# Kernel optimization log

Hardware: AMD Instinct MI355X
Metric: run time of the kernel (lower is better)

The kernel has to match this reference:

```python
import jax, jax.numpy as jnp
import numpy as np

N, D, E = 100000, 128, 1600000
C = 1.0
MIN_NORM = 1e-15   # hgcn min_norm clamp
BALL_EPS = 4e-3    # float32 eps for proj onto Poincare ball


def artanh(x):
    # hgcn Artanh clamps input away from +-1 (use 1e-7, the fp32-representable analog of 1e-15)
    return jnp.arctanh(jnp.clip(x, -1.0 + 1e-7, 1.0 - 1e-7))


def _norm(x):
    return jnp.maximum(jnp.linalg.norm(x, axis=-1, keepdims=True), MIN_NORM)


def proj(x, c):
    norm = _norm(x)
    maxnorm = (1.0 - BALL_EPS) / jnp.sqrt(c)
    return jnp.where(norm > maxnorm, x / norm * maxnorm, x)


def expmap0(u, c):
    sc = jnp.sqrt(c)
    n = _norm(u)
    return jnp.tanh(sc * n) * u / (sc * n)


def logmap0(p, c):
    sc = jnp.sqrt(c)
    n = _norm(p)
    return artanh(sc * n) * p / (sc * n)


def mobius_add(x, y, c):
    x2 = jnp.sum(x * x, -1, keepdims=True)
    y2 = jnp.sum(y * y, -1, keepdims=True)
    xy = jnp.sum(x * y, -1, keepdims=True)
    num = (1.0 + 2.0 * c * xy + c * y2) * x + (1.0 - c * x2) * y
    den = 1.0 + 2.0 * c * xy + c * c * x2 * y2
    return num / jnp.maximum(den, MIN_NORM)


def mobius_matvec(m, x, c):
    sc = jnp.sqrt(c)
    xn = _norm(x)
    mx = x @ m.T
    mxn = _norm(mx)
    res = jnp.tanh(mxn / xn * artanh(sc * xn)) * mx / (mxn * sc)
    zero = jnp.all(mx == 0, axis=-1, keepdims=True)
    return jnp.where(zero, jnp.zeros_like(res), res)


def hgc_layer(x, edge_index, edge_weight, w, b, c_in, c_out, n):
    # HypLinear: mobius matvec + hyperbolic bias
    h = proj(mobius_matvec(w, x, c_in), c_in)
    hyp_b = proj(expmap0(b[None, :], c_in), c_in)
    h = proj(mobius_add(h, hyp_b, c_in), c_in)
    # HypAgg: aggregate in tangent space via sparse adjacency (spmm)
    xt = logmap0(h, c_in)                                   # [N, D]
    msg = xt[edge_index[1]] * edge_weight[:, None]          # [E, D]
    agg = jax.ops.segment_sum(msg, edge_index[0], num_segments=n)
    h = proj(expmap0(agg, c_in), c_in)
    # HypAct: relu in tangent space, re-map to ball at c_out
    xt = jax.nn.relu(logmap0(h, c_in))
    return proj(expmap0(xt, c_out), c_out)


def setup_inputs() -> dict:
    key = jax.random.key(0)
    ks = jax.random.split(key, 8)
    x = jax.random.normal(ks[0], (N, D), dtype=jnp.float32)
    edge_index = jax.random.randint(ks[1], (2, E), 0, N, dtype=jnp.int64 if jax.config.jax_enable_x64 else jnp.int32)
    edge_weight = jax.random.uniform(ks[2], (E,), dtype=jnp.float32)
    s = 1.0 / np.sqrt(D)
    w1 = jax.random.normal(ks[3], (D, D), dtype=jnp.float32) * s
    b1 = jax.random.normal(ks[4], (D,), dtype=jnp.float32) * s
    w2 = jax.random.normal(ks[5], (D, D), dtype=jnp.float32) * s
    b2 = jax.random.normal(ks[6], (D,), dtype=jnp.float32) * s
    return {"x": x, "edge_index": edge_index, "edge_weight": edge_weight,
            "w1": w1, "b1": b1, "w2": w2, "b2": b2}


def reference(x, edge_index, edge_weight, w1, b1, w2, b2):
    c = jnp.float32(C)
    n = x.shape[0]
    # encode(): proj_tan0 is identity on the Poincare ball
    xh = proj(expmap0(x, c), c)
    h = hgc_layer(xh, edge_index, edge_weight, w1, b1, c, c, n)
    h = hgc_layer(h, edge_index, edge_weight, w2, b2, c, c, n)
    return h
```

## Files before the change

### kernel.cpp

```cpp
#include <hip/hip_runtime.h>
#include <math.h>
#include <stdint.h>

#define D 128
#define MAXNORM (1.0f - 4e-3f)
#define ART_CLAMP 0.9999999f
#define BKT_BITS 7
#define BKT_NODES 128
#define BKT_CAP 4096

typedef __attribute__((ext_vector_type(8))) short short8;
typedef __attribute__((ext_vector_type(4))) float float4v;
typedef __attribute__((ext_vector_type(4))) int intv4;

__device__ __forceinline__ float waveAllReduce(float v) {
#pragma unroll
    for (int off = 32; off; off >>= 1) v += __shfl_xor(v, off, 64);
    return v;
}

__device__ __forceinline__ float reduce16(float v) {
    v += __shfl_xor(v, 8, 64);
    v += __shfl_xor(v, 4, 64);
    v += __shfl_xor(v, 2, 64);
    v += __shfl_xor(v, 1, 64);
    return v;
}

__device__ __forceinline__ uint16_t f2bf(float f) {
    uint32_t u = __float_as_uint(f);
    uint32_t r = u + 0x7FFFu + ((u >> 16) & 1u);
    return (uint16_t)(r >> 16);
}
__device__ __forceinline__ float bf2f(uint16_t b) {
    return __uint_as_float((uint32_t)b << 16);
}

__device__ __forceinline__ float rcpf(float x) { return __builtin_amdgcn_rcpf(x); }
__device__ __forceinline__ float fsqrtf(float x) { return __builtin_amdgcn_sqrtf(x); }
__device__ __forceinline__ float fast_tanh(float x) {
    float e = __expf(2.0f * x);
    float t = 1.0f - 2.0f * rcpf(e + 1.0f);
    return (x < 1e-4f) ? x : t;
}
__device__ __forceinline__ float fast_atanh(float x) {
    float t = 0.5f * __logf((1.0f + x) * rcpf(1.0f - x));
    return (x < 1e-4f) ? x : t;
}


__global__ __launch_bounds__(64) void biasKernel(const float* __restrict__ B1,
                                                 const float* __restrict__ B2,
                                                 float* __restrict__ HBOUT) {
    int lane = threadIdx.x;
    const float* B = blockIdx.x ? B2 : B1;
    float v0 = B[lane], v1 = B[lane + 64];
    float nn = fmaxf(sqrtf(waveAllReduce(v0 * v0 + v1 * v1)), 1e-15f);
    float t = tanhf(nn);
    float sc = t / nn;
    float pn = fmaxf(t, 1e-15f);
    if (pn > MAXNORM) sc *= MAXNORM / pn;
    HBOUT[blockIdx.x * D + lane] = v0 * sc;
    HBOUT[blockIdx.x * D + lane + 64] = v1 * sc;
}


__global__ __launch_bounds__(256) void prepW(const float* __restrict__ W1,
                                             const float* __restrict__ W2,
                                             uint16_t* __restrict__ Whi1,
                                             uint16_t* __restrict__ Wlo1,
                                             uint16_t* __restrict__ Whi2,
                                             uint16_t* __restrict__ Wlo2) {
    int i = blockIdx.x * 256 + threadIdx.x;
    float a1 = W1[i];
    uint16_t h1 = f2bf(a1);
    Whi1[i] = h1;
    Wlo1[i] = f2bf(a1 - bf2f(h1));
    float a2 = W2[i];
    uint16_t h2 = f2bf(a2);
    Whi2[i] = h2;
    Wlo2[i] = f2bf(a2 - bf2f(h2));
}


__global__ __launch_bounds__(256) void rowNorms(const float* __restrict__ X,
                                                float* __restrict__ XN, int n) {
    int lane = threadIdx.x & 63;
    int wv = (blockIdx.x * 256 + threadIdx.x) >> 6;
    int nw = (gridDim.x * 256) >> 6;
    for (int r = wv; r < n; r += nw) {
        float2 v = *(const float2*)(X + (size_t)r * D + lane * 2);
        float nn = sqrtf(waveAllReduce(v.x * v.x + v.y * v.y));
        if (lane == 0) XN[r] = nn;
    }
}


__global__ __launch_bounds__(256) void bucketHisto(const int* __restrict__ DST,
                                                   int* __restrict__ bcnt, int E, int B) {
    __shared__ int cnt[1024];
    int tid = threadIdx.x;
    for (int i = tid; i < B; i += 256) cnt[i] = 0;
    __syncthreads();
    int start = blockIdx.x * 8192;
    int endE = min(start + 8192, E);
    for (int e = start + tid; e < endE; e += 256)
        atomicAdd(&cnt[DST[e] >> BKT_BITS], 1);
    __syncthreads();
    for (int i = tid; i < B; i += 256)
        if (cnt[i]) atomicAdd(&bcnt[i], cnt[i]);
}

__global__ __launch_bounds__(1024) void bucketScan(const int* __restrict__ bcnt,
                                                   int* __restrict__ boff,
                                                   int* __restrict__ gcur,
                                                   int* __restrict__ rp_last,
                                                   int B, int E) {
    __shared__ int sd[1024];
    int tid = threadIdx.x;
    int v = (tid < B) ? bcnt[tid] : 0;
    sd[tid] = v;
    __syncthreads();
    for (int off = 1; off < 1024; off <<= 1) {
        int t = (tid >= off) ? sd[tid - off] : 0;
        __syncthreads();
        sd[tid] += t;
        __syncthreads();
    }
    int ex = sd[tid] - v;
    if (tid < B) { boff[tid] = ex; gcur[tid] = ex; }
    if (tid == 0) { boff[B] = E; *rp_last = E; }
}

__global__ __launch_bounds__(256) void binEdges(const int* __restrict__ DST,
                                                const int* __restrict__ SRC,
                                                const float* __restrict__ EW,
                                                int* __restrict__ gcur,
                                                int2* __restrict__ binned, int E, int B) {
    __shared__ int cnt[1024];
    __shared__ int base[1024];
    int tid = threadIdx.x;
    int start = blockIdx.x * 8192;
    int endE = min(start + 8192, E);
    for (int i = tid; i < B; i += 256) cnt[i] = 0;
    __syncthreads();
    for (int e = start + tid; e < endE; e += 256)
        atomicAdd(&cnt[DST[e] >> BKT_BITS], 1);
    __syncthreads();
    for (int i = tid; i < B; i += 256) {
        int c = cnt[i];
        base[i] = (c > 0) ? atomicAdd(&gcur[i], c) : 0;
        cnt[i] = 0;
    }
    __syncthreads();
    for (int e = start + tid; e < endE; e += 256) {
        int d = DST[e];
        int bk = d >> BKT_BITS;
        int r = atomicAdd(&cnt[bk], 1);
        binned[base[bk] + r] =
            make_int2(SRC[e] | ((d & (BKT_NODES - 1)) << 24), __float_as_int(EW[e]));
    }
}


__global__ __launch_bounds__(256) void perBucketSort(int2* __restrict__ binned,
                                                     const int* __restrict__ boff,
                                                     int* __restrict__ rp, int n) {
    __shared__ int cnt[BKT_NODES];
    __shared__ int cur[BKT_NODES];
    __shared__ int2 buf[BKT_CAP];
    int tid = threadIdx.x;
    int b = blockIdx.x;
    int beg = boff[b], end = boff[b + 1];

    if (tid < BKT_NODES) cnt[tid] = 0;
    __syncthreads();
    for (int e = beg + tid; e < end; e += 256)
        atomicAdd(&cnt[((uint32_t)binned[e].x) >> 24], 1);
    __syncthreads();
    int v = (tid < BKT_NODES) ? cnt[tid] : 0;
    if (tid < BKT_NODES) cur[tid] = v;
    __syncthreads();
    for (int off = 1; off < BKT_NODES; off <<= 1) {
        int t = (tid < BKT_NODES && tid >= off) ? cur[tid - off] : 0;
        __syncthreads();
        if (tid < BKT_NODES) cur[tid] += t;
        __syncthreads();
    }
    if (tid < BKT_NODES) {
        int ex = cur[tid] - v;
        int g = b * BKT_NODES + tid;
        if (g < n) rp[g] = beg + ex;
        cur[tid] = ex;
    }
    __syncthreads();
    for (int e = beg + tid; e < end; e += 256) {
        int2 pr = binned[e];
        int dl = ((uint32_t)pr.x) >> 24;
        int pos = atomicAdd(&cur[dl], 1);
        if (pos < BKT_CAP) buf[pos] = make_int2(pr.x & 0x00FFFFFF, pr.y);
    }
    __syncthreads();
    int cnt_tot = end - beg;
    for (int i = tid; i < cnt_tot && i < BKT_CAP; i += 256)
        binned[beg + i] = buf[i];
}


__device__ __forceinline__ void split8(const float* v, short8* hi, short8* lo) {
    union { uint32_t u[4]; short8 s; } H, L;
#pragma unroll
    for (int i = 0; i < 4; i++) {
        uint16_t h0 = f2bf(v[2 * i]), h1 = f2bf(v[2 * i + 1]);
        uint16_t l0 = f2bf(v[2 * i] - bf2f(h0));
        uint16_t l1 = f2bf(v[2 * i + 1] - bf2f(h1));
        H.u[i] = (uint32_t)h0 | ((uint32_t)h1 << 16);
        L.u[i] = (uint32_t)l0 | ((uint32_t)l1 << 16);
    }
    *hi = H.s;
    *lo = L.s;
}

#define CS_STRIDE 136

template <bool ENCODE>
__global__ __launch_bounds__(256, 3) void gemmM(const float* __restrict__ A,
                                                const uint16_t* __restrict__ Whi,
                                                const uint16_t* __restrict__ Wlo,
                                                const float* __restrict__ XN,
                                                const float* __restrict__ HB,
                                                uint16_t* __restrict__ XT, int n) {
    __shared__ short8 Ah[2][16][16];
    __shared__ short8 Al[2][16][16];
    __shared__ float Cs[16 * CS_STRIDE];
    int tid = threadIdx.x;
    int lane = tid & 63;
    int wv = tid >> 6;
    int tx = lane & 15;
    int q = lane >> 4;
    int sw = tx & 7;
    int row0 = blockIdx.x * 64;

    short8 wh[2][4], wl[2][4];
#pragma unroll
    for (int c = 0; c < 2; c++) {
        int wrow = 16 * (2 * wv + c) + tx;
        const uint16_t* ph = Whi + (size_t)wrow * D + q * 8;
        const uint16_t* pl = Wlo + (size_t)wrow * D + q * 8;
#pragma unroll
        for (int t = 0; t < 4; t++) {
            wh[c][t] = *(const short8*)(ph + t * 32);
            wl[c][t] = *(const short8*)(pl + t * 32);
        }
    }

    float hbf[8];
#pragma unroll
    for (int c = 0; c < 8; c++) hbf[c] = HB[16 * c + tx];
    float hbsq = 0.f;
#pragma unroll
    for (int c = 0; c < 8; c++) hbsq += hbf[c] * hbf[c];
    float hb2 = reduce16(hbsq);

    auto loadA = [&](int tau, float4& v0, float4& v1) {
        int gr = row0 + tau * 16 + tx;
        if (gr >= n) gr = n - 1;
        const float4* ap = (const float4*)(A + (size_t)gr * D + wv * 32 + q * 8);
        v0 = ap[0];
        v1 = ap[1];
    };
    auto splitStore = [&](int b, float4 v0, float4 v1) {
        float v[8] = {v0.x, v0.y, v0.z, v0.w, v1.x, v1.y, v1.z, v1.w};
        short8 hi, lo;
        split8(v, &hi, &lo);
        int pch = (4 * wv + q) ^ sw;
        Ah[b][tx][pch] = hi;
        Al[b][tx][pch] = lo;
    };

    float4 pa0, pa1;
    loadA(0, pa0, pa1);
    splitStore(0, pa0, pa1);
    loadA(1, pa0, pa1);
    __syncthreads();

#pragma unroll
    for (int tau = 0; tau < 4; tau++) {
        int b = tau & 1;
        float4v acc[2];
        acc[0] = (float4v){0.f, 0.f, 0.f, 0.f};
        acc[1] = (float4v){0.f, 0.f, 0.f, 0.f};
#pragma unroll
        for (int t = 0; t < 4; t++) {
            int pch = (4 * t + q) ^ sw;
            short8 ahi = Ah[b][tx][pch];
            short8 alo = Al[b][tx][pch];
#pragma unroll
            for (int c = 0; c < 2; c++) {
                acc[c] = __builtin_amdgcn_mfma_f32_16x16x32_bf16(ahi, wh[c][t], acc[c], 0, 0, 0);
                acc[c] = __builtin_amdgcn_mfma_f32_16x16x32_bf16(ahi, wl[c][t], acc[c], 0, 0, 0);
                acc[c] = __builtin_amdgcn_mfma_f32_16x16x32_bf16(alo, wh[c][t], acc[c], 0, 0, 0);
            }
        }

#pragma unroll
        for (int c = 0; c < 2; c++) {
            int col = 16 * (2 * wv + c) + tx;
#pragma unroll
            for (int p = 0; p < 4; p++) {
                int lr = 4 * q + p;
                Cs[lr * CS_STRIDE + ((col + 4 * lr) & 127)] = acc[c][p];
            }
        }

        if (tau < 3) {
            splitStore(b ^ 1, pa0, pa1);
            if (tau < 2) loadA(tau + 2, pa0, pa1);
        }
        __syncthreads();

        int lr = 4 * wv + q;
        int row = row0 + tau * 16 + lr;
        if (row < n) {
            float y[8];
#pragma unroll
            for (int c = 0; c < 8; c++)
                y[c] = Cs[lr * CS_STRIDE + ((16 * c + tx + 4 * lr) & 127)];

            float s = 0.f;
#pragma unroll
            for (int c = 0; c < 8; c++) s += y[c] * y[c];
            float yn2 = reduce16(s);
            float sc, xns;
            if (ENCODE) {
                float nn = fmaxf(XN[row], 1e-15f);
                float t = fast_tanh(nn);
                sc = t * rcpf(nn);
                float pn = fmaxf(t, 1e-15f);
                if (pn > MAXNORM) { sc *= MAXNORM * rcpf(pn); pn = MAXNORM; }
                xns = pn;
            } else {
                sc = 1.0f;
                xns = fmaxf(XN[row], 1e-15f);
            }
            float mxn2 = sc * sc * yn2;
            float mxn = fmaxf(fsqrtf(mxn2), 1e-15f);
            float arg = (mxn * rcpf(xns)) * fast_atanh(fminf(xns, ART_CLAMP));
            float t = fast_tanh(arg);
            float s2 = (mxn2 == 0.0f) ? 0.0f : (sc * t * rcpf(mxn));
            float h[8];
#pragma unroll
            for (int c = 0; c < 8; c++) h[c] = y[c] * s2;
            float rn = fmaxf(t, 1e-15f);
            float hn = rn;
            if (rn > MAXNORM) {
                float f = MAXNORM * rcpf(rn);
#pragma unroll
                for (int c = 0; c < 8; c++) h[c] *= f;
                hn = MAXNORM;
            }
            float x2 = hn * hn;
            float d0 = 0.f;
#pragma unroll
            for (int c = 0; c < 8; c++) d0 += h[c] * hbf[c];
            float xy = reduce16(d0);
            float k1 = 1.0f + 2.0f * xy + hb2;
            float k2 = 1.0f - x2;
            float den = fmaxf(1.0f + 2.0f * xy + x2 * hb2, 1e-15f);
            float rden = rcpf(den);
            float av[8];
            float s3 = 0.f;
#pragma unroll
            for (int c = 0; c < 8; c++) {
                av[c] = (k1 * h[c] + k2 * hbf[c]) * rden;
                s3 += av[c] * av[c];
            }
            float an = fmaxf(fsqrtf(reduce16(s3)), 1e-15f);
            float fproj = 1.0f;
            if (an > MAXNORM) { fproj = MAXNORM * rcpf(an); an = MAXNORM; }
            float lm = fproj * fast_atanh(fminf(an, ART_CLAMP)) * rcpf(an);
            uint16_t* o = XT + (size_t)row * D + tx;
#pragma unroll
            for (int c = 0; c < 8; c++) o[16 * c] = f2bf(av[c] * lm);
        }
        __syncthreads();
    }
}


template <bool STORE_HN>
__global__ __launch_bounds__(256) void aggC(const uint16_t* __restrict__ XT,
                                            const int* __restrict__ rp,
                                            const int2* __restrict__ sorted,
                                            float* __restrict__ OUT,
                                            float* __restrict__ HN, int n) {
    int tid = threadIdx.x;
    int lane = tid & 63;
    int q = lane >> 4;
    int tx = lane & 15;
    int wv = (blockIdx.x * 256 + tid) >> 6;
    int g = wv * 4 + q;
    bool valid = (g < n);
    int gc = valid ? g : (n - 1);
    uint32_t beg = (uint32_t)rp[gc];
    uint32_t end = valid ? (uint32_t)rp[gc + 1] : beg;
    uint32_t deg = end - beg;

    int m = (int)deg;
    m = max(m, __shfl_xor(m, 16, 64));
    m = max(m, __shfl_xor(m, 32, 64));
    int ms = __builtin_amdgcn_readfirstlane(m);

    const char* sbase = (const char*)sorted;
    const char* xbase = (const char*)XT;
    uint32_t txoff = (uint32_t)tx * 16u;
    uint32_t jb = beg * 8u;
    uint32_t jendb = end * 8u;
    uint32_t jlastb = (jendb > 0u) ? (jendb - 8u) : 0u;

    float a[8];
#pragma unroll
    for (int c = 0; c < 8; c++) a[c] = 0.f;

    int2 e0 = *(const int2*)(sbase + min(jb, jlastb));
    int2 e1 = *(const int2*)(sbase + min(jb + 8u, jlastb));
    int2 e2 = *(const int2*)(sbase + min(jb + 16u, jlastb));
    int2 e3 = *(const int2*)(sbase + min(jb + 24u, jlastb));
    for (int i = 0; i < ms; i += 4) {
        int2 f0 = *(const int2*)(sbase + min(jb + 32u, jlastb));
        int2 f1 = *(const int2*)(sbase + min(jb + 40u, jlastb));
        int2 f2 = *(const int2*)(sbase + min(jb + 48u, jlastb));
        int2 f3 = *(const int2*)(sbase + min(jb + 56u, jlastb));
        intv4 u0 = *(const intv4*)(xbase + ((((uint32_t)e0.x) << 8) + txoff));
        intv4 u1 = *(const intv4*)(xbase + ((((uint32_t)e1.x) << 8) + txoff));
        intv4 u2 = *(const intv4*)(xbase + ((((uint32_t)e2.x) << 8) + txoff));
        intv4 u3 = *(const intv4*)(xbase + ((((uint32_t)e3.x) << 8) + txoff));
        float w0 = (jb < jendb) ? __int_as_float(e0.y) : 0.f;
        float w1 = (jb + 8u < jendb) ? __int_as_float(e1.y) : 0.f;
        float w2 = (jb + 16u < jendb) ? __int_as_float(e2.y) : 0.f;
        float w3 = (jb + 24u < jendb) ? __int_as_float(e3.y) : 0.f;
#pragma unroll
        for (int k = 0; k < 4; k++) {
            a[2 * k]     = fmaf(__uint_as_float(((uint32_t)u0[k]) << 16), w0, a[2 * k]);
            a[2 * k + 1] = fmaf(__uint_as_float(((uint32_t)u0[k]) & 0xFFFF0000u), w0, a[2 * k + 1]);
        }
#pragma unroll
        for (int k = 0; k < 4; k++) {
            a[2 * k]     = fmaf(__uint_as_float(((uint32_t)u1[k]) << 16), w1, a[2 * k]);
            a[2 * k + 1] = fmaf(__uint_as_float(((uint32_t)u1[k]) & 0xFFFF0000u), w1, a[2 * k + 1]);
        }
#pragma unroll
        for (int k = 0; k < 4; k++) {
            a[2 * k]     = fmaf(__uint_as_float(((uint32_t)u2[k]) << 16), w2, a[2 * k]);
            a[2 * k + 1] = fmaf(__uint_as_float(((uint32_t)u2[k]) & 0xFFFF0000u), w2, a[2 * k + 1]);
        }
#pragma unroll
        for (int k = 0; k < 4; k++) {
            a[2 * k]     = fmaf(__uint_as_float(((uint32_t)u3[k]) << 16), w3, a[2 * k]);
            a[2 * k + 1] = fmaf(__uint_as_float(((uint32_t)u3[k]) & 0xFFFF0000u), w3, a[2 * k + 1]);
        }
        jb += 32u;
        e0 = f0; e1 = f1; e2 = f2; e3 = f3;
    }

    float ss = 0.f;
#pragma unroll
    for (int c = 0; c < 8; c++) ss += a[c] * a[c];
    float nn = fmaxf(fsqrtf(reduce16(ss)), 1e-15f);
    float t = fast_tanh(nn);
    float sc = t * rcpf(nn);
    float pn = fmaxf(t, 1e-15f);
    if (pn > MAXNORM) { sc *= MAXNORM * rcpf(pn); pn = MAXNORM; }
    float lm = fast_atanh(fminf(pn, ART_CLAMP)) * rcpf(pn);
    float r[8];
    float ss2 = 0.f;
#pragma unroll
    for (int c = 0; c < 8; c++) {
        r[c] = fmaxf(lm * sc * a[c], 0.f);
        ss2 += r[c] * r[c];
    }
    float rn = fmaxf(fsqrtf(reduce16(ss2)), 1e-15f);
    float t2 = fast_tanh(rn);
    float sc2 = t2 * rcpf(rn);
    float on = fmaxf(t2, 1e-15f);
    if (on > MAXNORM) { sc2 *= MAXNORM * rcpf(on); on = MAXNORM; }
    if (valid) {
        float4* o = (float4*)(OUT + (size_t)g * D + tx * 8);
        o[0] = make_float4(r[0] * sc2, r[1] * sc2, r[2] * sc2, r[3] * sc2);
        o[1] = make_float4(r[4] * sc2, r[5] * sc2, r[6] * sc2, r[7] * sc2);
        if (STORE_HN && tx == 0) HN[g] = on;
    }
}


extern "C" void kernel_launch(void* const* d_in, const int* in_sizes, int n_in,
                              void* d_out, int out_size, void* d_ws, size_t ws_size,
                              hipStream_t stream) {
    const float* x  = (const float*)d_in[0];
    const int*   ei = (const int*)d_in[1];
    const float* ew = (const float*)d_in[2];
    const float* w1 = (const float*)d_in[3];
    const float* b1 = (const float*)d_in[4];
    const float* w2 = (const float*)d_in[5];
    const float* b2 = (const float*)d_in[6];
    int n = in_sizes[0] / D;
    int E = in_sizes[2];
    int B = (n + BKT_NODES - 1) >> BKT_BITS;

    uint16_t* xtb = (uint16_t*)d_ws;
    int*   bcnt = (int*)(xtb + (size_t)n * D);
    int*   boff = bcnt + 1024;
    int*   gcur = boff + 1025;
    int*   rp   = gcur + 1024;
    float* xn   = (float*)(rp + n + 1);
    uint16_t* whi1 = (uint16_t*)(((uintptr_t)(xn + n) + 15) & ~(uintptr_t)15);
    uint16_t* wlo1 = whi1 + 128 * 128;
    uint16_t* whi2 = wlo1 + 128 * 128;
    uint16_t* wlo2 = whi2 + 128 * 128;
    float* hb = (float*)(wlo2 + 128 * 128);
    uintptr_t p = (uintptr_t)(hb + 2 * D);
    int2* binned = (int2*)((p + 15) & ~(uintptr_t)15);
    float* Hd = (float*)d_out;

    const int* dst = ei;
    const int* src = ei + E;

    const int gE8 = (E + 8191) / 8192;
    const int gG = (n + 63) / 64;
    const int gAgg = (n + 15) / 16;

    biasKernel<<<2, 64, 0, stream>>>(b1, b2, hb);
    prepW<<<64, 256, 0, stream>>>(w1, w2, whi1, wlo1, whi2, wlo2);
    rowNorms<<<1024, 256, 0, stream>>>(x, xn, n);

    hipMemsetAsync(bcnt, 0, 1024 * sizeof(int), stream);
    bucketHisto<<<gE8, 256, 0, stream>>>(dst, bcnt, E, B);
    bucketScan<<<1, 1024, 0, stream>>>(bcnt, boff, gcur, rp + n, B, E);
    binEdges<<<gE8, 256, 0, stream>>>(dst, src, ew, gcur, binned, E, B);
    perBucketSort<<<B, 256, 0, stream>>>(binned, boff, rp, n);

    gemmM<true><<<gG, 256, 0, stream>>>(x, whi1, wlo1, xn, hb, xtb, n);
    aggC<true><<<gAgg, 256, 0, stream>>>(xtb, rp, binned, Hd, xn, n);

    gemmM<false><<<gG, 256, 0, stream>>>(Hd, whi2, wlo2, xn, hb + D, xtb, n);
    aggC<false><<<gAgg, 256, 0, stream>>>(xtb, rp, binned, (float*)d_out, nullptr, n);
}
```

Before: 403.4 us.

## Fuse preprocessing kernels and overlap edge binning/sorting with first GEMM

Merges rowNorms, bucket histogram, weight split and bias setup into one launch with block-index dispatch. The first-layer GEMM is split across two launches and co-scheduled with the edge binning and per-bucket sort kernels, since those phases do not depend on each other. The aim is to cut launch gaps and fill idle CUs during the low-parallelism graph preprocessing. The cost is a shared-memory union that raises per-block LDS to the larger of the two uses, plus heterogeneous blocks inside one grid.

```diff
diff --git a/kernel.cpp b/kernel.cpp
--- a/kernel.cpp
+++ b/kernel.cpp
@@ -8,6 +8,7 @@
 #define BKT_BITS 7
 #define BKT_NODES 128
 #define BKT_CAP 4096
+#define NB_ROWN 1024
 
 typedef __attribute__((ext_vector_type(8))) short short8;
 typedef __attribute__((ext_vector_type(4))) float float4v;
@@ -49,29 +50,55 @@
 }
 
 
-__global__ __launch_bounds__(64) void biasKernel(const float* __restrict__ B1,
-                                                 const float* __restrict__ B2,
-                                                 float* __restrict__ HBOUT) {
-    int lane = threadIdx.x;
-    const float* B = blockIdx.x ? B2 : B1;
-    float v0 = B[lane], v1 = B[lane + 64];
-    float nn = fmaxf(sqrtf(waveAllReduce(v0 * v0 + v1 * v1)), 1e-15f);
-    float t = tanhf(nn);
-    float sc = t / nn;
-    float pn = fmaxf(t, 1e-15f);
-    if (pn > MAXNORM) sc *= MAXNORM / pn;
-    HBOUT[blockIdx.x * D + lane] = v0 * sc;
-    HBOUT[blockIdx.x * D + lane + 64] = v1 * sc;
-}
-
-
-__global__ __launch_bounds__(256) void prepW(const float* __restrict__ W1,
-                                             const float* __restrict__ W2,
-                                             uint16_t* __restrict__ Whi1,
-                                             uint16_t* __restrict__ Wlo1,
-                                             uint16_t* __restrict__ Whi2,
-                                             uint16_t* __restrict__ Wlo2) {
-    int i = blockIdx.x * 256 + threadIdx.x;
+#define CS_STRIDE 136
+
+struct GemmLds {
+    short8 Ah[2][16][16];
+    short8 Al[2][16][16];
+    float Cs[16 * CS_STRIDE];
+};
+struct BinLds { int cnt[1024]; int base[1024]; };
+struct SortLds { int cnt[BKT_NODES]; int cur[BKT_NODES]; int2 buf[BKT_CAP]; };
+union LdsBG { GemmLds g; BinLds b; };
+union LdsSG { GemmLds g; SortLds s; };
+
+
+__device__ __forceinline__ void rowNorms_body(int bid, int tid,
+                                              const float* __restrict__ X,
+                                              float* __restrict__ XN, int n) {
+    int lane = tid & 63;
+    int wv = (bid * 256 + tid) >> 6;
+    const int nw = (NB_ROWN * 256) >> 6;
+    for (int r = wv; r < n; r += nw) {
+        float2 v = *(const float2*)(X + (size_t)r * D + lane * 2);
+        float nn = sqrtf(waveAllReduce(v.x * v.x + v.y * v.y));
+        if (lane == 0) XN[r] = nn;
+    }
+}
+
+__device__ __forceinline__ void histo_body(int bid, int tid,
+                                           const int* __restrict__ DST,
+                                           int* __restrict__ bcnt, int E, int B,
+                                           int* cnt) {
+    for (int i = tid; i < B; i += 256) cnt[i] = 0;
+    __syncthreads();
+    int start = bid * 8192;
+    int endE = min(start + 8192, E);
+    for (int e = start + tid; e < endE; e += 256)
+        atomicAdd(&cnt[DST[e] >> BKT_BITS], 1);
+    __syncthreads();
+    for (int i = tid; i < B; i += 256)
+        if (cnt[i]) atomicAdd(&bcnt[i], cnt[i]);
+}
+
+__device__ __forceinline__ void prepW_body(int bid, int tid,
+                                           const float* __restrict__ W1,
+                                           const float* __restrict__ W2,
+                                           uint16_t* __restrict__ Whi1,
+                                           uint16_t* __restrict__ Wlo1,
+                                           uint16_t* __restrict__ Whi2,
+                                           uint16_t* __restrict__ Wlo2) {
+    int i = bid * 256 + tid;
     float a1 = W1[i];
     uint16_t h1 = f2bf(a1);
     Whi1[i] = h1;
@@ -82,65 +109,31 @@
     Wlo2[i] = f2bf(a2 - bf2f(h2));
 }
 
-
-__global__ __launch_bounds__(256) void rowNorms(const float* __restrict__ X,
-                                                float* __restrict__ XN, int n) {
-    int lane = threadIdx.x & 63;
-    int wv = (blockIdx.x * 256 + threadIdx.x) >> 6;
-    int nw = (gridDim.x * 256) >> 6;
-    for (int r = wv; r < n; r += nw) {
-        float2 v = *(const float2*)(X + (size_t)r * D + lane * 2);
-        float nn = sqrtf(waveAllReduce(v.x * v.x + v.y * v.y));
-        if (lane == 0) XN[r] = nn;
-    }
-}
-
-
-__global__ __launch_bounds__(256) void bucketHisto(const int* __restrict__ DST,
-                                                   int* __restrict__ bcnt, int E, int B) {
-    __shared__ int cnt[1024];
-    int tid = threadIdx.x;
-    for (int i = tid; i < B; i += 256) cnt[i] = 0;
-    __syncthreads();
-    int start = blockIdx.x * 8192;
-    int endE = min(start + 8192, E);
-    for (int e = start + tid; e < endE; e += 256)
-        atomicAdd(&cnt[DST[e] >> BKT_BITS], 1);
-    __syncthreads();
-    for (int i = tid; i < B; i += 256)
-        if (cnt[i]) atomicAdd(&bcnt[i], cnt[i]);
-}
-
-__global__ __launch_bounds__(1024) void bucketScan(const int* __restrict__ bcnt,
-                                                   int* __restrict__ boff,
-                                                   int* __restrict__ gcur,
-                                                   int* __restrict__ rp_last,
-                                                   int B, int E) {
-    __shared__ int sd[1024];
-    int tid = threadIdx.x;
-    int v = (tid < B) ? bcnt[tid] : 0;
-    sd[tid] = v;
-    __syncthreads();
-    for (int off = 1; off < 1024; off <<= 1) {
-        int t = (tid >= off) ? sd[tid - off] : 0;
-        __syncthreads();
-        sd[tid] += t;
-        __syncthreads();
-    }
-    int ex = sd[tid] - v;
-    if (tid < B) { boff[tid] = ex; gcur[tid] = ex; }
-    if (tid == 0) { boff[B] = E; *rp_last = E; }
-}
-
-__global__ __launch_bounds__(256) void binEdges(const int* __restrict__ DST,
-                                                const int* __restrict__ SRC,
-                                                const float* __restrict__ EW,
-                                                int* __restrict__ gcur,
-                                                int2* __restrict__ binned, int E, int B) {
-    __shared__ int cnt[1024];
-    __shared__ int base[1024];
-    int tid = threadIdx.x;
-    int start = blockIdx.x * 8192;
+__device__ __forceinline__ void bias_body(int bid, int tid,
+                                          const float* __restrict__ B1,
+                                          const float* __restrict__ B2,
+                                          float* __restrict__ HBOUT) {
+    if (tid >= 64) return;
+    int lane = tid;
+    const float* Bp = bid ? B2 : B1;
+    float v0 = Bp[lane], v1 = Bp[lane + 64];
+    float nn = fmaxf(sqrtf(waveAllReduce(v0 * v0 + v1 * v1)), 1e-15f);
+    float t = tanhf(nn);
+    float sc = t / nn;
+    float pn = fmaxf(t, 1e-15f);
+    if (pn > MAXNORM) sc *= MAXNORM / pn;
+    HBOUT[bid * D + lane] = v0 * sc;
+    HBOUT[bid * D + lane + 64] = v1 * sc;
+}
+
+__device__ __forceinline__ void binEdges_body(int bid, int tid,
+                                              const int* __restrict__ DST,
+                                              const int* __restrict__ SRC,
+                                              const float* __restrict__ EW,
+                                              int* __restrict__ gcur,
+                                              int2* __restrict__ binned, int E, int B,
+                                              int* cnt, int* base) {
+    int start = bid * 8192;
     int endE = min(start + 8192, E);
     for (int i = tid; i < B; i += 256) cnt[i] = 0;
     __syncthreads();
@@ -162,17 +155,12 @@
     }
 }
 
-
-__global__ __launch_bounds__(256) void perBucketSort(int2* __restrict__ binned,
-                                                     const int* __restrict__ boff,
-                                                     int* __restrict__ rp, int n) {
-    __shared__ int cnt[BKT_NODES];
-    __shared__ int cur[BKT_NODES];
-    __shared__ int2 buf[BKT_CAP];
-    int tid = threadIdx.x;
-    int b = blockIdx.x;
+__device__ __forceinline__ void sort_body(int b, int tid,
+                                          int2* __restrict__ binned,
+                                          const int* __restrict__ boff,
+                                          int* __restrict__ rp, int n,
+                                          int* cnt, int* cur, int2* buf) {
     int beg = boff[b], end = boff[b + 1];
-
     if (tid < BKT_NODES) cnt[tid] = 0;
     __syncthreads();
     for (int e = beg + tid; e < end; e += 256)
@@ -221,25 +209,21 @@
     *lo = L.s;
 }
 
-#define CS_STRIDE 136
-
 template <bool ENCODE>
-__global__ __launch_bounds__(256, 3) void gemmM(const float* __restrict__ A,
-                                                const uint16_t* __restrict__ Whi,
-                                                const uint16_t* __restrict__ Wlo,
-                                                const float* __restrict__ XN,
-                                                const float* __restrict__ HB,
-                                                uint16_t* __restrict__ XT, int n) {
-    __shared__ short8 Ah[2][16][16];
-    __shared__ short8 Al[2][16][16];
-    __shared__ float Cs[16 * CS_STRIDE];
-    int tid = threadIdx.x;
+__device__ __forceinline__ void gemm_body(int gbid, int rowOff, int tid,
+                                          const float* __restrict__ A,
+                                          const uint16_t* __restrict__ Whi,
+                                          const uint16_t* __restrict__ Wlo,
+                                          const float* __restrict__ XN,
+                                          const float* __restrict__ HB,
+                                          uint16_t* __restrict__ XT, int n,
+                                          GemmLds* L) {
     int lane = tid & 63;
     int wv = tid >> 6;
     int tx = lane & 15;
     int q = lane >> 4;
     int sw = tx & 7;
-    int row0 = blockIdx.x * 64;
+    int row0 = rowOff + gbid * 64;
 
     short8 wh[2][4], wl[2][4];
 #pragma unroll
@@ -274,8 +258,8 @@
         short8 hi, lo;
         split8(v, &hi, &lo);
         int pch = (4 * wv + q) ^ sw;
-        Ah[b][tx][pch] = hi;
-        Al[b][tx][pch] = lo;
+        L->Ah[b][tx][pch] = hi;
+        L->Al[b][tx][pch] = lo;
     };
 
     float4 pa0, pa1;
@@ -293,8 +277,8 @@
 #pragma unroll
         for (int t = 0; t < 4; t++) {
             int pch = (4 * t + q) ^ sw;
-            short8 ahi = Ah[b][tx][pch];
-            short8 alo = Al[b][tx][pch];
+            short8 ahi = L->Ah[b][tx][pch];
+            short8 alo = L->Al[b][tx][pch];
 #pragma unroll
             for (int c = 0; c < 2; c++) {
                 acc[c] = __builtin_amdgcn_mfma_f32_16x16x32_bf16(ahi, wh[c][t], acc[c], 0, 0, 0);
@@ -309,7 +293,7 @@
 #pragma unroll
             for (int p = 0; p < 4; p++) {
                 int lr = 4 * q + p;
-                Cs[lr * CS_STRIDE + ((col + 4 * lr) & 127)] = acc[c][p];
+                L->Cs[lr * CS_STRIDE + ((col + 4 * lr) & 127)] = acc[c][p];
             }
         }
 
@@ -325,7 +309,7 @@
             float y[8];
 #pragma unroll
             for (int c = 0; c < 8; c++)
-                y[c] = Cs[lr * CS_STRIDE + ((16 * c + tx + 4 * lr) & 127)];
+                y[c] = L->Cs[lr * CS_STRIDE + ((16 * c + tx + 4 * lr) & 127)];
 
             float s = 0.f;
 #pragma unroll
@@ -388,6 +372,89 @@
 }
 
 
+__global__ __launch_bounds__(256) void fusedPre(
+    const float* __restrict__ X, float* __restrict__ XN, int n,
+    const int* __restrict__ DST, int* __restrict__ bcnt, int E, int B, int gH,
+    const float* __restrict__ W1, const float* __restrict__ W2,
+    uint16_t* __restrict__ Whi1, uint16_t* __restrict__ Wlo1,
+    uint16_t* __restrict__ Whi2, uint16_t* __restrict__ Wlo2,
+    const float* __restrict__ B1, const float* __restrict__ B2,
+    float* __restrict__ HBOUT) {
+    __shared__ int cnt[1024];
+    int bid = blockIdx.x, tid = threadIdx.x;
+    if (bid < NB_ROWN) {
+        rowNorms_body(bid, tid, X, XN, n);
+    } else if (bid < NB_ROWN + gH) {
+        histo_body(bid - NB_ROWN, tid, DST, bcnt, E, B, cnt);
+    } else if (bid < NB_ROWN + gH + 64) {
+        prepW_body(bid - NB_ROWN - gH, tid, W1, W2, Whi1, Wlo1, Whi2, Wlo2);
+    } else {
+        bias_body(bid - NB_ROWN - gH - 64, tid, B1, B2, HBOUT);
+    }
+}
+
+__global__ __launch_bounds__(1024) void bucketScan(const int* __restrict__ bcnt,
+                                                   int* __restrict__ boff,
+                                                   int* __restrict__ gcur,
+                                                   int* __restrict__ rp_last,
+                                                   int B, int E) {
+    __shared__ int sd[1024];
+    int tid = threadIdx.x;
+    int v = (tid < B) ? bcnt[tid] : 0;
+    sd[tid] = v;
+    __syncthreads();
+    for (int off = 1; off < 1024; off <<= 1) {
+        int t = (tid >= off) ? sd[tid - off] : 0;
+        __syncthreads();
+        sd[tid] += t;
+        __syncthreads();
+    }
+    int ex = sd[tid] - v;
+    if (tid < B) { boff[tid] = ex; gcur[tid] = ex; }
+    if (tid == 0) { boff[B] = E; *rp_last = E; }
+}
+
+__global__ __launch_bounds__(256, 3) void fusedBinGemm(
+    const int* __restrict__ DST, const int* __restrict__ SRC,
+    const float* __restrict__ EW, int* __restrict__ gcur,
+    int2* __restrict__ binned, int E, int B, int gBin,
+    const float* __restrict__ A, const uint16_t* __restrict__ Whi,
+    const uint16_t* __restrict__ Wlo, const float* __restrict__ XN,
+    const float* __restrict__ HB, uint16_t* __restrict__ XT, int n) {
+    __shared__ LdsBG u;
+    int bid = blockIdx.x, tid = threadIdx.x;
+    if (bid < gBin)
+        binEdges_body(bid, tid, DST, SRC, EW, gcur, binned, E, B, u.b.cnt, u.b.base);
+    else
+        gemm_body<true>(bid - gBin, 0, tid, A, Whi, Wlo, XN, HB, XT, n, &u.g);
+}
+
+__global__ __launch_bounds__(256, 3) void fusedSortGemm(
+    int2* __restrict__ binned, const int* __restrict__ boff,
+    int* __restrict__ rp, int n, int gSort,
+    const float* __restrict__ A, const uint16_t* __restrict__ Whi,
+    const uint16_t* __restrict__ Wlo, const float* __restrict__ XN,
+    const float* __restrict__ HB, uint16_t* __restrict__ XT, int rowOff) {
+    __shared__ LdsSG u;
+    int bid = blockIdx.x, tid = threadIdx.x;
+    if (bid < gSort)
+        sort_body(bid, tid, binned, boff, rp, n, u.s.cnt, u.s.cur, u.s.buf);
+    else
+        gemm_body<true>(bid - gSort, rowOff, tid, A, Whi, Wlo, XN, HB, XT, n, &u.g);
+}
+
+template <bool ENCODE>
+__global__ __launch_bounds__(256, 3) void gemmM(const float* __restrict__ A,
+                                                const uint16_t* __restrict__ Whi,
+                                                const uint16_t* __restrict__ Wlo,
+                                                const float* __restrict__ XN,
+                                                const float* __restrict__ HB,
+                                                uint16_t* __restrict__ XT, int n) {
+    __shared__ GemmLds L;
+    gemm_body<ENCODE>(blockIdx.x, 0, threadIdx.x, A, Whi, Wlo, XN, HB, XT, n, &L);
+}
+
+
 template <bool STORE_HN>
 __global__ __launch_bounds__(256) void aggC(const uint16_t* __restrict__ XT,
                                             const int* __restrict__ rp,
@@ -527,21 +594,27 @@
 
     const int gE8 = (E + 8191) / 8192;
     const int gG = (n + 63) / 64;
+    const int GA = min(256, gG);
+    const int GB = gG - GA;
     const int gAgg = (n + 15) / 16;
 
-    biasKernel<<<2, 64, 0, stream>>>(b1, b2, hb);
-    prepW<<<64, 256, 0, stream>>>(w1, w2, whi1, wlo1, whi2, wlo2);
-    rowNorms<<<1024, 256, 0, stream>>>(x, xn, n);
-
     hipMemsetAsync(bcnt, 0, 1024 * sizeof(int), stream);
-    bucketHisto<<<gE8, 256, 0, stream>>>(dst, bcnt, E, B);
+
+    fusedPre<<<NB_ROWN + gE8 + 64 + 2, 256, 0, stream>>>(
+        x, xn, n, dst, bcnt, E, B, gE8,
+        w1, w2, whi1, wlo1, whi2, wlo2, b1, b2, hb);
+
     bucketScan<<<1, 1024, 0, stream>>>(bcnt, boff, gcur, rp + n, B, E);
-    binEdges<<<gE8, 256, 0, stream>>>(dst, src, ew, gcur, binned, E, B);
-    perBucketSort<<<B, 256, 0, stream>>>(binned, boff, rp, n);
-
-    gemmM<true><<<gG, 256, 0, stream>>>(x, whi1, wlo1, xn, hb, xtb, n);
+
+    fusedBinGemm<<<gE8 + GA, 256, 0, stream>>>(
+        dst, src, ew, gcur, binned, E, B, gE8,
+        x, whi1, wlo1, xn, hb, xtb, n);
+
+    fusedSortGemm<<<B + GB, 256, 0, stream>>>(
+        binned, boff, rp, n, B,
+        x, whi1, wlo1, xn, hb, xtb, GA * 64);
+
     aggC<true><<<gAgg, 256, 0, stream>>>(xtb, rp, binned, Hd, xn, n);
-
     gemmM<false><<<gG, 256, 0, stream>>>(Hd, whi2, wlo2, xn, hb + D, xtb, n);
     aggC<false><<<gAgg, 256, 0, stream>>>(xtb, rp, binned, (float*)d_out, nullptr, n);
 }
```

Measured after the change: 382.7 us. -5.1%, faster.
